# Kernel tuning notes

Hardware: AMD Instinct MI355X
Metric: run time of the kernel (lower is better)

Reference implementation:

```python
import jax, jax.numpy as jnp
import numpy as np
import math

B, D, P = 32768, 4096, 16

def setup_inputs() -> dict:
    key = jax.random.key(0)
    ks = jax.random.split(key, 4)
    x = jax.random.normal(ks[0], (B, D), dtype=jnp.float32)
    # orthogonal-ish init: random normal rows scaled (exact orthogonality not needed for correctness baseline)
    W_refine = jax.random.normal(ks[1], (P, D), dtype=jnp.float32) / np.sqrt(D)
    W_out = jax.random.normal(ks[2], (P, D), dtype=jnp.float32) / np.sqrt(D)
    b_refine = jnp.zeros((P,), dtype=jnp.float32)
    b_out = jnp.zeros((P,), dtype=jnp.float32)
    gamma = jnp.ones((D,), dtype=jnp.float32)
    beta = jnp.zeros((D,), dtype=jnp.float32)
    return {"x": x, "W_refine": W_refine, "b_refine": b_refine,
            "W_out": W_out, "b_out": b_out, "gamma": gamma, "beta": beta}

def reference(x, W_refine, b_refine, W_out, b_out, gamma, beta):
    # phases in (-pi, pi)
    refine_phase = jnp.tanh(x @ W_refine.T + b_refine) * math.pi   # [B, P]
    output_phase = jnp.tanh(x @ W_out.T + b_out) * math.pi        # [B, P]
    # Since x is real: Re(e^{i r} * x * e^{-i o}) = x * cos(r - o)
    # phase_alignment = Re(e^{i(r-o)}) = cos(r - o)
    cosd = jnp.cos(refine_phase - output_phase)                    # [B, P]
    resonance = jnp.mean(cosd, axis=-1, keepdims=True)             # [B, 1]
    resonance_gain = jax.nn.softplus(resonance + 0.5)              # [B, 1]
    # summed = sum_p Re(bound_p * conj(output_phasor_p)) = x * sum_p cos(r_p - o_p)
    summed = x * jnp.sum(cosd, axis=-1, keepdims=True)             # [B, D]
    n_planes = W_refine.shape[0]
    output = summed * resonance_gain / n_planes                    # [B, D]
    # LayerNorm(output) with eps=1e-5 (torch default)
    mu = jnp.mean(output, axis=-1, keepdims=True)
    var = jnp.mean((output - mu) ** 2, axis=-1, keepdims=True)
    normed = (output - mu) * jax.lax.rsqrt(var + 1e-5) * gamma + beta
    return x + normed
```

## Files before the change

### kernel.cpp

```cpp
#include <hip/hip_runtime.h>
#include <math.h>


constexpr int Dh     = 4096;
constexpr int Ph     = 16;
constexpr int NPL    = 32;
constexpr int CHUNK  = 256;
constexpr int NCHUNK = Dh / CHUNK;
constexpr int RPB    = 8;
constexpr int NW     = 8;
constexpr int PPW    = NPL / NW;
constexpr int BLOCK  = 64 * NW;

__device__ __forceinline__ float4 gload_s(const float* sbase, int voff) {
    float4 v;
    asm volatile("global_load_dwordx4 %0, %1, %2"
                 : "=v"(v) : "v"(voff), "s"(sbase));
    return v;
}

__device__ __forceinline__ float4 gload_v(const float* addr) {
    float4 v;
    asm volatile("global_load_dwordx4 %0, %1, off"
                 : "=v"(v) : "v"(addr));
    return v;
}

__global__ __launch_bounds__(BLOCK, 2)
void phase_fused(const float* __restrict__ x,
                 const float* __restrict__ Wr,
                 const float* __restrict__ br,
                 const float* __restrict__ Wo,
                 const float* __restrict__ bo,
                 const float* __restrict__ gamma,
                 const float* __restrict__ beta,
                 float* __restrict__ out)
{
    __shared__ float dots_lds[RPB][NPL];
    __shared__ float stats_lds[RPB][2];
    __shared__ float scale_lds[RPB][2];

    const int t    = threadIdx.x;
    const int wv   = t >> 6;
    const int lane = t & 63;
    const size_t rowbase = (size_t)blockIdx.x * RPB;

    const float* xbase[RPB];
#pragma unroll
    for (int r = 0; r < RPB; ++r)
        xbase[r] = x + (rowbase + r) * (size_t)Dh;

    const float* wptr[PPW];
#pragma unroll
    for (int p = 0; p < PPW; ++p) {
        const int q = wv * PPW + p;
        wptr[p] = ((q < Ph) ? (Wr + (size_t)q * Dh) : (Wo + (size_t)(q - Ph) * Dh))
                  + lane * 4;
    }

    float acc[RPB][PPW];
#pragma unroll
    for (int r = 0; r < RPB; ++r)
#pragma unroll
        for (int p = 0; p < PPW; ++p) acc[r][p] = 0.f;
    float sx = 0.f, sxx = 0.f;

    int voff = lane * 16;
#pragma unroll 1
    for (int c = 0; c < NCHUNK; ++c) {
        float4 x4[RPB];
#pragma unroll
        for (int r = 0; r < RPB; ++r)
            x4[r] = gload_s(xbase[r], voff);
        float4 w4[PPW];
#pragma unroll
        for (int p = 0; p < PPW; ++p)
            w4[p] = gload_v(wptr[p]);

        asm volatile("s_waitcnt vmcnt(0)" ::: "memory");
        __builtin_amdgcn_sched_barrier(0);

#pragma unroll
        for (int r = 0; r < RPB; ++r) {
            if (r == wv) {
                sx  += x4[r].x + x4[r].y + x4[r].z + x4[r].w;
                sxx += x4[r].x*x4[r].x + x4[r].y*x4[r].y
                     + x4[r].z*x4[r].z + x4[r].w*x4[r].w;
            }
#pragma unroll
            for (int p = 0; p < PPW; ++p)
                acc[r][p] += x4[r].x*w4[p].x + x4[r].y*w4[p].y
                           + x4[r].z*w4[p].z + x4[r].w*w4[p].w;
        }
        voff += CHUNK * 4;
#pragma unroll
        for (int p = 0; p < PPW; ++p) wptr[p] += CHUNK;
    }

#pragma unroll
    for (int r = 0; r < RPB; ++r)
#pragma unroll
        for (int p = 0; p < PPW; ++p) {
            float v = acc[r][p];
#pragma unroll
            for (int m = 1; m < 64; m <<= 1) v += __shfl_xor(v, m, 64);
            if (lane == 0) dots_lds[r][wv * PPW + p] = v;
        }
#pragma unroll
    for (int m = 1; m < 64; m <<= 1) {
        sx  += __shfl_xor(sx, m, 64);
        sxx += __shfl_xor(sxx, m, 64);
    }
    if (lane == 0) { stats_lds[wv][0] = sx; stats_lds[wv][1] = sxx; }
    __syncthreads();

    if (t < RPB * Ph) {
        const int r = t >> 4, p = t & 15;
        float d1 = dots_lds[r][p]      + br[p];
        float d2 = dots_lds[r][Ph + p] + bo[p];
        float cd = cosf((tanhf(d1) - tanhf(d2)) * 3.14159265358979323846f);
#pragma unroll
        for (int m = 1; m < 16; m <<= 1) cd += __shfl_xor(cd, m, 16);
        if (p == 0) {
            float s    = cd;
            float gain = log1pf(expf(s * (1.f / Ph) + 0.5f));
            float cm   = s * gain * (1.f / Ph);
            float mu   = stats_lds[r][0] * (1.f / Dh);
            float var  = stats_lds[r][1] * (1.f / Dh) - mu * mu;
            var = fmaxf(var, 0.f);
            float rstd  = rsqrtf(cm * cm * var + 1e-5f);
            float alpha = cm * rstd;
            scale_lds[r][0] = alpha;
            scale_lds[r][1] = alpha * mu;
        }
    }
    __syncthreads();

    {
        const int col0 = wv * 512 + lane * 4;
        const float4 g4a = *(const float4*)(gamma + col0);
        const float4 g4b = *(const float4*)(gamma + col0 + 256);
        const float4 b4a = *(const float4*)(beta  + col0);
        const float4 b4b = *(const float4*)(beta  + col0 + 256);
#pragma unroll
        for (int r = 0; r < RPB; ++r) {
            const float alpha = scale_lds[r][0];
            const float am    = scale_lds[r][1];
            const float* xr  = x   + (rowbase + r) * (size_t)Dh;
            float*       orw = out + (rowbase + r) * (size_t)Dh;
            float4 xa = *(const float4*)(xr + col0);
            float4 xb = *(const float4*)(xr + col0 + 256);
            float4 oa, ob;
            oa.x = xa.x + g4a.x * (alpha * xa.x - am) + b4a.x;
            oa.y = xa.y + g4a.y * (alpha * xa.y - am) + b4a.y;
            oa.z = xa.z + g4a.z * (alpha * xa.z - am) + b4a.z;
            oa.w = xa.w + g4a.w * (alpha * xa.w - am) + b4a.w;
            ob.x = xb.x + g4b.x * (alpha * xb.x - am) + b4b.x;
            ob.y = xb.y + g4b.y * (alpha * xb.y - am) + b4b.y;
            ob.z = xb.z + g4b.z * (alpha * xb.z - am) + b4b.z;
            ob.w = xb.w + g4b.w * (alpha * xb.w - am) + b4b.w;
            *(float4*)(orw + col0)       = oa;
            *(float4*)(orw + col0 + 256) = ob;
        }
    }
}

extern "C" void kernel_launch(void* const* d_in, const int* in_sizes, int n_in,
                              void* d_out, int out_size, void* d_ws, size_t ws_size,
                              hipStream_t stream)
{
    const float* x     = (const float*)d_in[0];
    const float* Wr    = (const float*)d_in[1];
    const float* br    = (const float*)d_in[2];
    const float* Wo    = (const float*)d_in[3];
    const float* bo    = (const float*)d_in[4];
    const float* gamma = (const float*)d_in[5];
    const float* beta  = (const float*)d_in[6];
    float* out = (float*)d_out;

    const int B = in_sizes[0] / Dh;
    dim3 grid(B / RPB);
    phase_fused<<<grid, BLOCK, 0, stream>>>(x, Wr, br, Wo, bo, gamma, beta, out);
}
```

Before: 386.0 us.

## Tile rows and projections 2D across waves with split wait for weight loads

Result: slower. 495.6 us (+28.4%).

```diff
diff --git a/kernel.cpp b/kernel.cpp
--- a/kernel.cpp
+++ b/kernel.cpp
@@ -7,17 +7,11 @@
 constexpr int NPL    = 32;
 constexpr int CHUNK  = 256;
 constexpr int NCHUNK = Dh / CHUNK;
-constexpr int RPB    = 8;
+constexpr int RPB    = 16;
 constexpr int NW     = 8;
-constexpr int PPW    = NPL / NW;
+constexpr int RW     = 8;
+constexpr int PW     = 8;
 constexpr int BLOCK  = 64 * NW;
-
-__device__ __forceinline__ float4 gload_s(const float* sbase, int voff) {
-    float4 v;
-    asm volatile("global_load_dwordx4 %0, %1, %2"
-                 : "=v"(v) : "v"(voff), "s"(sbase));
-    return v;
-}
 
 __device__ __forceinline__ float4 gload_v(const float* addr) {
     float4 v;
@@ -26,7 +20,7 @@
     return v;
 }
 
-__global__ __launch_bounds__(BLOCK, 2)
+__global__ __launch_bounds__(BLOCK, 1)
 void phase_fused(const float* __restrict__ x,
                  const float* __restrict__ Wr,
                  const float* __restrict__ br,
@@ -43,75 +37,95 @@
     const int t    = threadIdx.x;
     const int wv   = t >> 6;
     const int lane = t & 63;
+    const int rg   = wv >> 2;
+    const int pg   = wv & 3;
     const size_t rowbase = (size_t)blockIdx.x * RPB;
 
-    const float* xbase[RPB];
+    const float* xptr[RW];
 #pragma unroll
-    for (int r = 0; r < RPB; ++r)
-        xbase[r] = x + (rowbase + r) * (size_t)Dh;
+    for (int r = 0; r < RW; ++r)
+        xptr[r] = x + (rowbase + rg * RW + r) * (size_t)Dh + lane * 4;
 
-    const float* wptr[PPW];
+    const float* wb = (pg < 2) ? (Wr + (size_t)(pg * 8) * Dh)
+                               : (Wo + (size_t)((pg - 2) * 8) * Dh);
+    const float* wptr[PW];
 #pragma unroll
-    for (int p = 0; p < PPW; ++p) {
-        const int q = wv * PPW + p;
-        wptr[p] = ((q < Ph) ? (Wr + (size_t)q * Dh) : (Wo + (size_t)(q - Ph) * Dh))
-                  + lane * 4;
-    }
+    for (int p = 0; p < PW; ++p)
+        wptr[p] = wb + (size_t)p * Dh + lane * 4;
 
-    float acc[RPB][PPW];
+    float acc[RW][PW];
 #pragma unroll
-    for (int r = 0; r < RPB; ++r)
+    for (int r = 0; r < RW; ++r)
 #pragma unroll
-        for (int p = 0; p < PPW; ++p) acc[r][p] = 0.f;
-    float sx = 0.f, sxx = 0.f;
+        for (int p = 0; p < PW; ++p) acc[r][p] = 0.f;
+    float sx[2]  = {0.f, 0.f};
+    float sxx[2] = {0.f, 0.f};
 
-    int voff = lane * 16;
 #pragma unroll 1
     for (int c = 0; c < NCHUNK; ++c) {
-        float4 x4[RPB];
+        float4 x4[RW];
 #pragma unroll
-        for (int r = 0; r < RPB; ++r)
-            x4[r] = gload_s(xbase[r], voff);
-        float4 w4[PPW];
+        for (int r = 0; r < RW; ++r) x4[r] = gload_v(xptr[r]);
+        float4 w4a[4];
 #pragma unroll
-        for (int p = 0; p < PPW; ++p)
-            w4[p] = gload_v(wptr[p]);
+        for (int p = 0; p < 4; ++p) w4a[p] = gload_v(wptr[p]);
+        float4 w4b[4];
+#pragma unroll
+        for (int p = 0; p < 4; ++p) w4b[p] = gload_v(wptr[4 + p]);
+
+        asm volatile("s_waitcnt vmcnt(4)" ::: "memory");
+        __builtin_amdgcn_sched_barrier(0);
+
+#pragma unroll
+        for (int r = 0; r < RW; ++r) {
+            if ((r >> 1) == pg) {
+                sx[r & 1]  += x4[r].x + x4[r].y + x4[r].z + x4[r].w;
+                sxx[r & 1] += x4[r].x*x4[r].x + x4[r].y*x4[r].y
+                            + x4[r].z*x4[r].z + x4[r].w*x4[r].w;
+            }
+#pragma unroll
+            for (int p = 0; p < 4; ++p)
+                acc[r][p] += x4[r].x*w4a[p].x + x4[r].y*w4a[p].y
+                           + x4[r].z*w4a[p].z + x4[r].w*w4a[p].w;
+        }
 
         asm volatile("s_waitcnt vmcnt(0)" ::: "memory");
         __builtin_amdgcn_sched_barrier(0);
 
 #pragma unroll
-        for (int r = 0; r < RPB; ++r) {
-            if (r == wv) {
-                sx  += x4[r].x + x4[r].y + x4[r].z + x4[r].w;
-                sxx += x4[r].x*x4[r].x + x4[r].y*x4[r].y
-                     + x4[r].z*x4[r].z + x4[r].w*x4[r].w;
-            }
+        for (int r = 0; r < RW; ++r)
 #pragma unroll
-            for (int p = 0; p < PPW; ++p)
-                acc[r][p] += x4[r].x*w4[p].x + x4[r].y*w4[p].y
-                           + x4[r].z*w4[p].z + x4[r].w*w4[p].w;
-        }
-        voff += CHUNK * 4;
+            for (int p = 0; p < 4; ++p)
+                acc[r][4 + p] += x4[r].x*w4b[p].x + x4[r].y*w4b[p].y
+                               + x4[r].z*w4b[p].z + x4[r].w*w4b[p].w;
+
 #pragma unroll
-        for (int p = 0; p < PPW; ++p) wptr[p] += CHUNK;
+        for (int r = 0; r < RW; ++r) xptr[r] += CHUNK;
+#pragma unroll
+        for (int p = 0; p < PW; ++p) wptr[p] += CHUNK;
     }
 
 #pragma unroll
-    for (int r = 0; r < RPB; ++r)
+    for (int r = 0; r < RW; ++r)
 #pragma unroll
-        for (int p = 0; p < PPW; ++p) {
+        for (int p = 0; p < PW; ++p) {
             float v = acc[r][p];
 #pragma unroll
             for (int m = 1; m < 64; m <<= 1) v += __shfl_xor(v, m, 64);
-            if (lane == 0) dots_lds[r][wv * PPW + p] = v;
+            if (lane == 0) dots_lds[rg * RW + r][pg * PW + p] = v;
         }
 #pragma unroll
-    for (int m = 1; m < 64; m <<= 1) {
-        sx  += __shfl_xor(sx, m, 64);
-        sxx += __shfl_xor(sxx, m, 64);
+    for (int i = 0; i < 2; ++i) {
+#pragma unroll
+        for (int m = 1; m < 64; m <<= 1) {
+            sx[i]  += __shfl_xor(sx[i], m, 64);
+            sxx[i] += __shfl_xor(sxx[i], m, 64);
+        }
+        if (lane == 0) {
+            stats_lds[rg * RW + 2 * pg + i][0] = sx[i];
+            stats_lds[rg * RW + 2 * pg + i][1] = sxx[i];
+        }
     }
-    if (lane == 0) { stats_lds[wv][0] = sx; stats_lds[wv][1] = sxx; }
     __syncthreads();
 
     if (t < RPB * Ph) {
@@ -142,7 +156,7 @@
         const float4 g4b = *(const float4*)(gamma + col0 + 256);
         const float4 b4a = *(const float4*)(beta  + col0);
         const float4 b4b = *(const float4*)(beta  + col0 + 256);
-#pragma unroll
+#pragma unroll 4
         for (int r = 0; r < RPB; ++r) {
             const float alpha = scale_lds[r][0];
             const float am    = scale_lds[r][1];
```
